# Kernel tuning notes

Hardware: AMD Instinct MI355X
Metric: run time of the kernel (lower is better)

## Reference

```python
import jax, jax.numpy as jnp
import numpy as np

B, T, P = 64, 512, 8
V, O, E, H, C_SIZE = 50000, 50000, 512, 2048, 5
A1, A2, A3, A4, A5 = 1.0, 0.5, 0.5, 0.5, 0.5


def setup_inputs() -> dict:
    key = jax.random.key(0)
    ks = jax.random.split(key, 8)
    s = 0.02
    return dict(
        encoder_output=jax.random.normal(ks[0], (B, H), jnp.float32),
        predict_sequence=jax.random.randint(ks[1], (B, P), 0, 500),
        source=jax.random.randint(ks[2], (B, T), 0, 500),
        source_lens=jax.random.randint(ks[3], (B,), T // 2, T + 1),
        E_table=jax.random.normal(ks[4], (V, E), jnp.float32) * s,
        W1=jax.random.normal(ks[5], (C_SIZE * E, H), jnp.float32) * s,
        b1=jnp.zeros((H,), jnp.float32),
        W2=jax.random.normal(ks[6], (H, O), jnp.float32) * s,
        b2=jnp.zeros((O,), jnp.float32),
        W3=jax.random.normal(ks[7], (H, O), jnp.float32) * s,
        b3=jnp.zeros((O,), jnp.float32),
    )


def _features(predict_sequence, source, source_lens):
    # Vectorized replacement of the per-sample Python n-gram/reorder loop.
    b, t = source.shape
    mask = jnp.arange(t)[None, :] < source_lens[:, None]          # valid positions [B,T]
    w1 = predict_sequence[:, -1]                                  # last predicted token
    w2a = predict_sequence[:, -2]                                 # second-to-last
    # bigram: exists p with source[p]==w1 and source[p+1]==source[pos]
    first2 = source[:, :-1] == w1[:, None]                        # [B,T-1]
    eq2 = source[:, :, None] == source[:, None, 1:]               # [B,T,T-1]
    big = jnp.any(eq2 & first2[:, None, :], axis=-1)              # [B,T]
    # trigram: exists p with source[p]==w2a, source[p+1]==w1, source[p+2]==source[pos]
    first3 = (source[:, :-2] == w2a[:, None]) & (source[:, 1:-1] == w1[:, None])
    eq3 = source[:, :, None] == source[:, None, 2:]               # [B,T,T-2]
    tri = jnp.any(eq3 & first3[:, None, :], axis=-1)
    # reordering: first index of source[pos] < first index of w1 (when w1 present)
    eqw = source == w1[:, None]
    in_list = jnp.any(eqw, axis=-1)
    kpos = jnp.argmax(eqw, axis=-1)                               # first occurrence of w1
    jpos = jnp.argmax(source[:, :, None] == source[:, None, :], axis=-1)  # first occ. of each id
    reo = in_list[:, None] & (jpos < kpos[:, None])
    rows = jnp.broadcast_to(jnp.arange(b)[:, None], (b, t))
    def scat(flags):
        return jnp.zeros((b, O), jnp.float32).at[rows, source].max((flags & mask).astype(jnp.float32))
    return scat(mask), scat(big), scat(tri), scat(reo)


def reference(encoder_output, predict_sequence, source, source_lens,
              E_table, W1, b1, W2, b2, W3, b3):
    bsz = encoder_output.shape[0]
    ctx = E_table[predict_sequence[:, -C_SIZE:]].reshape(bsz, -1)  # [B, C*E]
    h = jnp.tanh(ctx @ W1 + b1)                                    # [B, H]
    out = (h @ W2 + b2) + (encoder_output @ W3 + b3)               # Vh + Wenc
    uni, big, tri, reo = _features(predict_sequence, source, source_lens)
    comb = out * A1 + uni * A2 + big * A3 + tri * A4 + reo * A5
    return jax.nn.softmax(comb, axis=1)
```

## Files before the change

### kernel.cpp

```cpp
#include <hip/hip_runtime.h>
#include <math.h>

#define BSZ   64
#define TLEN  512
#define ODIM  50000
#define HDIM  2048
#define K1DIM 2560
#define K2DIM 4096
#define KSPLIT 5

typedef __bf16 bf16x8 __attribute__((ext_vector_type(8)));
typedef float f32x4 __attribute__((ext_vector_type(4)));

__device__ __forceinline__ unsigned short f2b(float f) {
    unsigned int u = __float_as_uint(f);
    u += 0x7FFFu + ((u >> 16) & 1u);
    return (unsigned short)(u >> 16);
}

__device__ __forceinline__ bf16x8 ld_bf16x8(const unsigned short* p) {
    union { uint4 u; bf16x8 v; } x;
    x.u = *reinterpret_cast<const uint4*>(p);
    return x.v;
}

__global__ __launch_bounds__(256) void prep_kernel(
    const float* __restrict__ enc, const int* __restrict__ ps,
    const float* __restrict__ Et, unsigned short* __restrict__ ctx,
    unsigned short* __restrict__ A2)
{
    int i = blockIdx.x * 256 + threadIdx.x;
    const int NE = BSZ * HDIM;
    if (i < NE) {
        int m = i >> 11, j = i & (HDIM - 1);
        A2[m * K2DIM + HDIM + j] = f2b(enc[i]);
    } else {
        int t = i - NE;
        int m = t / K1DIM, j = t - m * K1DIM;
        int c = j >> 9, e = j & 511;
        int tok = ps[m * 8 + 3 + c];
        ctx[m * K1DIM + j] = f2b(Et[(size_t)tok * 512 + e]);
    }
}

__global__ __launch_bounds__(256) void gemm1_kernel(
    const unsigned short* __restrict__ Actx, const float* __restrict__ W1,
    float* __restrict__ part)
{
    int n0 = blockIdx.x * 64;
    int ks = blockIdx.y;
    int wave = threadIdx.x >> 6;
    int lane = threadIdx.x & 63;
    int q = lane >> 4, l16 = lane & 15;
    int ncol = n0 + wave * 16 + l16;

    f32x4 acc[4] = {};
    for (int kk = 0; kk < 16; ++kk) {
        int kq = ks * 512 + kk * 32 + q * 8;
        const unsigned short* ap = Actx + l16 * K1DIM + kq;
        bf16x8 a0 = ld_bf16x8(ap);
        bf16x8 a1 = ld_bf16x8(ap + 16 * K1DIM);
        bf16x8 a2 = ld_bf16x8(ap + 32 * K1DIM);
        bf16x8 a3 = ld_bf16x8(ap + 48 * K1DIM);
        const float* wp = W1 + (size_t)kq * HDIM + ncol;
        union { unsigned short s[8]; bf16x8 v; } bb;
#pragma unroll
        for (int j = 0; j < 8; ++j) { bb.s[j] = f2b(*wp); wp += HDIM; }
        acc[0] = __builtin_amdgcn_mfma_f32_16x16x32_bf16(a0, bb.v, acc[0], 0, 0, 0);
        acc[1] = __builtin_amdgcn_mfma_f32_16x16x32_bf16(a1, bb.v, acc[1], 0, 0, 0);
        acc[2] = __builtin_amdgcn_mfma_f32_16x16x32_bf16(a2, bb.v, acc[2], 0, 0, 0);
        acc[3] = __builtin_amdgcn_mfma_f32_16x16x32_bf16(a3, bb.v, acc[3], 0, 0, 0);
    }
    float* pp = part + (size_t)ks * (BSZ * HDIM);
#pragma unroll
    for (int mt = 0; mt < 4; ++mt)
#pragma unroll
        for (int r = 0; r < 4; ++r)
            pp[(mt * 16 + q * 4 + r) * HDIM + ncol] = acc[mt][r];
}

__global__ __launch_bounds__(256) void htanh_kernel(
    const float* __restrict__ part, const float* __restrict__ b1,
    unsigned short* __restrict__ A2)
{
    int i = blockIdx.x * 256 + threadIdx.x;
    int m = i >> 11, n = i & (HDIM - 1);
    float s = b1[n];
#pragma unroll
    for (int ks = 0; ks < KSPLIT; ++ks) s += part[(size_t)ks * (BSZ * HDIM) + m * HDIM + n];
    A2[m * K2DIM + n] = f2b(tanhf(s));
}

#define KT 64
#define SKB 136
#define BUFB (KT * SKB)

__global__ __launch_bounds__(256) void gemm2_kernel(
    const unsigned short* __restrict__ A, const float* __restrict__ W2,
    const float* __restrict__ W3, const float* __restrict__ b2,
    const float* __restrict__ b3, float* __restrict__ out)
{
    __shared__ char lds[2 * BUFB];
    int bid = blockIdx.x;
    int tile = (bid & 7) * 98 + (bid >> 3);
    if (tile >= 782) return;
    int n0 = tile * 64;

    int tid = threadIdx.x;
    int wave = tid >> 6;
    int lane = tid & 63;
    int q = lane >> 4, l16 = lane & 15;
    int ncol = n0 + wave * 16 + l16;
    int nloc = wave * 16 + l16;

    int rr = tid >> 4;
    int cg = tid & 15;
    int gcol = n0 + cg * 4;
    if (gcol > ODIM - 4) gcol = ODIM - 4;

    float4 Sa[4], Sb[4];
    f32x4 acc[4] = {};
    const unsigned short* abase = A + l16 * K2DIM;
    char* buf0 = lds;
    char* buf1 = lds + BUFB;

#define ISSUE(S, ktile) do {                                                  \
    int kg0 = (ktile) * KT;                                                   \
    _Pragma("unroll")                                                         \
    for (int r = 0; r < 4; ++r) {                                             \
        int krow = kg0 + r * 16 + rr;                                         \
        const float* srcp = (krow < HDIM) ? (W2 + (size_t)krow * ODIM)        \
                                          : (W3 + (size_t)(krow - HDIM) * ODIM); \
        S[r] = *reinterpret_cast<const float4*>(srcp + gcol);                 \
    } } while (0)

#define CONVERT(S, bufc) do {                                                 \
    _Pragma("unroll")                                                         \
    for (int r = 0; r < 4; ++r) {                                             \
        union { unsigned short s[4]; unsigned long long u; } pk;              \
        pk.s[0] = f2b(S[r].x); pk.s[1] = f2b(S[r].y);                         \
        pk.s[2] = f2b(S[r].z); pk.s[3] = f2b(S[r].w);                         \
        *reinterpret_cast<unsigned long long*>((bufc) + (r * 16 + rr) * SKB + cg * 8) = pk.u; \
    } } while (0)

#define COMPUTE(bufc, ktile) do {                                             \
    _Pragma("unroll")                                                         \
    for (int h = 0; h < 2; ++h) {                                             \
        int kq = (ktile) * KT + h * 32 + q * 8;                               \
        const unsigned short* ap = abase + kq;                                \
        bf16x8 a0 = ld_bf16x8(ap);                                            \
        bf16x8 a1 = ld_bf16x8(ap + 16 * K2DIM);                               \
        bf16x8 a2 = ld_bf16x8(ap + 32 * K2DIM);                               \
        bf16x8 a3 = ld_bf16x8(ap + 48 * K2DIM);                               \
        union { unsigned short s[8]; bf16x8 v; } bb;                          \
        const char* bp = (bufc) + (h * 32 + q * 8) * SKB + nloc * 2;          \
        _Pragma("unroll")                                                     \
        for (int j = 0; j < 8; ++j)                                           \
            bb.s[j] = *reinterpret_cast<const unsigned short*>(bp + j * SKB); \
        acc[0] = __builtin_amdgcn_mfma_f32_16x16x32_bf16(a0, bb.v, acc[0], 0, 0, 0); \
        acc[1] = __builtin_amdgcn_mfma_f32_16x16x32_bf16(a1, bb.v, acc[1], 0, 0, 0); \
        acc[2] = __builtin_amdgcn_mfma_f32_16x16x32_bf16(a2, bb.v, acc[2], 0, 0, 0); \
        acc[3] = __builtin_amdgcn_mfma_f32_16x16x32_bf16(a3, bb.v, acc[3], 0, 0, 0); \
    } } while (0)

#define BARRIER do {                                                          \
    asm volatile("s_waitcnt lgkmcnt(0)" ::: "memory");                        \
    __builtin_amdgcn_s_barrier();                                             \
} while (0)

    ISSUE(Sa, 0);
    ISSUE(Sb, 1);
    asm volatile("s_waitcnt vmcnt(4)" ::: "memory");
    CONVERT(Sa, buf0);
    BARRIER;

    for (int kt = 0; kt < 62; kt += 2) {
        ISSUE(Sa, kt + 2);
        asm volatile("s_waitcnt vmcnt(4)" ::: "memory");
        CONVERT(Sb, buf1);
        COMPUTE(buf0, kt);
        BARRIER;

        ISSUE(Sb, kt + 3);
        asm volatile("s_waitcnt vmcnt(4)" ::: "memory");
        CONVERT(Sa, buf0);
        COMPUTE(buf1, kt + 1);
        BARRIER;
    }
    asm volatile("s_waitcnt vmcnt(0)" ::: "memory");
    CONVERT(Sb, buf1);
    COMPUTE(buf0, 62);
    BARRIER;
    COMPUTE(buf1, 63);

#undef ISSUE
#undef CONVERT
#undef COMPUTE
#undef BARRIER

    if (ncol < ODIM) {
        float bias = b2[ncol] + b3[ncol];
#pragma unroll
        for (int mt = 0; mt < 4; ++mt)
#pragma unroll
            for (int r = 0; r < 4; ++r)
                out[(size_t)(mt * 16 + q * 4 + r) * ODIM + ncol] = acc[mt][r] + bias;
    }
}

__global__ __launch_bounds__(256) void feats_kernel(
    const int* __restrict__ src_g, const int* __restrict__ lens,
    const int* __restrict__ ps, float* __restrict__ out)
{
    __shared__ int src[TLEN];
    int b = blockIdx.x;
    int tid = threadIdx.x;
    for (int t = tid; t < TLEN; t += 256) src[t] = src_g[b * TLEN + t];
    __syncthreads();
    int len = lens[b];
    int w1 = ps[b * 8 + 7];
    int w2a = ps[b * 8 + 6];

    for (int t = tid; t < TLEN; t += 256) {
        int v = src[t];
        bool first = true, big = false, tri = false;
        int kp = TLEN;
        for (int j = 0; j < TLEN; ++j) {
            int sj = src[j];
            int sj1 = (j < TLEN - 1) ? src[j + 1] : -1;
            int sj2 = (j < TLEN - 2) ? src[j + 2] : -1;
            if (j < t && sj == v) first = false;
            if (sj == w1 && sj1 == v) big = true;
            if (sj == w2a && sj1 == w1 && sj2 == v) tri = true;
            if (sj == w1 && j < kp) kp = j;
        }
        if (t < len && first) {
            bool in_list = kp < TLEN;
            bool reo = in_list && (t < kp);
            float add = 0.5f * (1.0f + (big ? 1.0f : 0.0f) + (tri ? 1.0f : 0.0f) + (reo ? 1.0f : 0.0f));
            out[(size_t)b * ODIM + v] += add;
        }
    }
}

__global__ __launch_bounds__(256) void rowstats_kernel(
    const float* __restrict__ out, float* __restrict__ stats)
{
    int b = blockIdx.x, tid = threadIdx.x;
    const float* row = out + (size_t)b * ODIM;
    float m = -INFINITY, s = 0.0f;
    for (int i = tid; i < ODIM; i += 256) {
        float x = row[i];
        if (x > m) { s = s * __expf(m - x) + 1.0f; m = x; }
        else s += __expf(x - m);
    }
    __shared__ float ms[256], ss[256];
    ms[tid] = m; ss[tid] = s;
    __syncthreads();
    for (int off = 128; off > 0; off >>= 1) {
        if (tid < off) {
            float m1 = ms[tid], s1 = ss[tid];
            float m2 = ms[tid + off], s2 = ss[tid + off];
            float M = fmaxf(m1, m2);
            ss[tid] = s1 * __expf(m1 - M) + s2 * __expf(m2 - M);
            ms[tid] = M;
        }
        __syncthreads();
    }
    if (tid == 0) { stats[b] = ms[0]; stats[64 + b] = ss[0]; }
}

__global__ __launch_bounds__(256) void norm_kernel(
    float* __restrict__ out, const float* __restrict__ stats)
{
    int i = blockIdx.x * 256 + threadIdx.x;
    int row = i / 12500;
    int off = i - row * 12500;
    float m = stats[row];
    float inv = 1.0f / stats[64 + row];
    float4* p = reinterpret_cast<float4*>(out + (size_t)row * ODIM) + off;
    float4 x = *p;
    x.x = __expf(x.x - m) * inv;
    x.y = __expf(x.y - m) * inv;
    x.z = __expf(x.z - m) * inv;
    x.w = __expf(x.w - m) * inv;
    *p = x;
}

extern "C" void kernel_launch(void* const* d_in, const int* in_sizes, int n_in,
                              void* d_out, int out_size, void* d_ws, size_t ws_size,
                              hipStream_t stream) {
    const float* enc  = (const float*)d_in[0];
    const int*   ps   = (const int*)d_in[1];
    const int*   src  = (const int*)d_in[2];
    const int*   lens = (const int*)d_in[3];
    const float* Et   = (const float*)d_in[4];
    const float* W1   = (const float*)d_in[5];
    const float* b1   = (const float*)d_in[6];
    const float* W2   = (const float*)d_in[7];
    const float* b2   = (const float*)d_in[8];
    const float* W3   = (const float*)d_in[9];
    const float* b3   = (const float*)d_in[10];
    float* out = (float*)d_out;

    char* ws = (char*)d_ws;
    unsigned short* ctx = (unsigned short*)(ws);
    unsigned short* A2  = (unsigned short*)(ws + 524288);
    float* part         = (float*)(ws + 1048576);
    float* stats        = (float*)(ws + 3801088);

    prep_kernel<<<1152, 256, 0, stream>>>(enc, ps, Et, ctx, A2);
    gemm1_kernel<<<dim3(32, KSPLIT), 256, 0, stream>>>(ctx, W1, part);
    htanh_kernel<<<512, 256, 0, stream>>>(part, b1, A2);
    gemm2_kernel<<<784, 256, 0, stream>>>(A2, W2, W3, b2, b3, out);
    feats_kernel<<<64, 256, 0, stream>>>(src, lens, ps, out);
    rowstats_kernel<<<64, 256, 0, stream>>>(out, stats);
    norm_kernel<<<3125, 256, 0, stream>>>(out, stats);
}
```

Baseline: 1.188 ms.

## Widen gemm2 tiles to 128 columns with swizzled LDS and split feats blocks

Gemm2 now has each block cover 128 output columns instead of 64, so every wave computes two 16-column MFMA subtiles and reuses its A fragments twice. The grid shrinks from 784 to 391 blocks and the tile-to-XCD mapping changes to match. The LDS row stride grows and an XOR swizzle is applied to the B tile to limit bank conflicts, and twice as many float4 loads are kept in flight per stage. Feats_kernel is split into 4 chunks per batch row across 256 blocks of 128 threads to spread its serial scan over more CUs. The trade-off is more registers and LDS per block, and with 391 blocks the MI355X's CUs may not all be filled.

```diff
diff --git a/kernel.cpp b/kernel.cpp
--- a/kernel.cpp
+++ b/kernel.cpp
@@ -92,7 +92,7 @@
 }
 
 #define KT 64
-#define SKB 136
+#define SKB 264
 #define BUFB (KT * SKB)
 
 __global__ __launch_bounds__(256) void gemm2_kernel(
@@ -102,24 +102,22 @@
 {
     __shared__ char lds[2 * BUFB];
     int bid = blockIdx.x;
-    int tile = (bid & 7) * 98 + (bid >> 3);
-    if (tile >= 782) return;
-    int n0 = tile * 64;
+    int xcd = bid & 7, idx = bid >> 3;
+    int tile = (xcd < 7 ? xcd * 49 : 343) + idx;
+    int n0 = tile * 128;
 
     int tid = threadIdx.x;
     int wave = tid >> 6;
     int lane = tid & 63;
     int q = lane >> 4, l16 = lane & 15;
-    int ncol = n0 + wave * 16 + l16;
-    int nloc = wave * 16 + l16;
-
-    int rr = tid >> 4;
-    int cg = tid & 15;
+
+    int rr = tid >> 5;
+    int cg = tid & 31;
     int gcol = n0 + cg * 4;
     if (gcol > ODIM - 4) gcol = ODIM - 4;
 
-    float4 Sa[4], Sb[4];
-    f32x4 acc[4] = {};
+    float4 Sa[8], Sb[8];
+    f32x4 acc[4][2] = {};
     const unsigned short* abase = A + l16 * K2DIM;
     char* buf0 = lds;
     char* buf1 = lds + BUFB;
@@ -127,20 +125,22 @@
 #define ISSUE(S, ktile) do {                                                  \
     int kg0 = (ktile) * KT;                                                   \
     _Pragma("unroll")                                                         \
-    for (int r = 0; r < 4; ++r) {                                             \
-        int krow = kg0 + r * 16 + rr;                                         \
+    for (int r8 = 0; r8 < 8; ++r8) {                                          \
+        int krow = kg0 + r8 * 8 + rr;                                         \
         const float* srcp = (krow < HDIM) ? (W2 + (size_t)krow * ODIM)        \
                                           : (W3 + (size_t)(krow - HDIM) * ODIM); \
-        S[r] = *reinterpret_cast<const float4*>(srcp + gcol);                 \
+        S[r8] = *reinterpret_cast<const float4*>(srcp + gcol);                \
     } } while (0)
 
 #define CONVERT(S, bufc) do {                                                 \
     _Pragma("unroll")                                                         \
-    for (int r = 0; r < 4; ++r) {                                             \
+    for (int r8 = 0; r8 < 8; ++r8) {                                          \
+        int row = r8 * 8 + rr;                                                \
         union { unsigned short s[4]; unsigned long long u; } pk;              \
-        pk.s[0] = f2b(S[r].x); pk.s[1] = f2b(S[r].y);                         \
-        pk.s[2] = f2b(S[r].z); pk.s[3] = f2b(S[r].w);                         \
-        *reinterpret_cast<unsigned long long*>((bufc) + (r * 16 + rr) * SKB + cg * 8) = pk.u; \
+        pk.s[0] = f2b(S[r8].x); pk.s[1] = f2b(S[r8].y);                       \
+        pk.s[2] = f2b(S[r8].z); pk.s[3] = f2b(S[r8].w);                       \
+        *reinterpret_cast<unsigned long long*>(                               \
+            (bufc) + row * SKB + ((cg * 8) ^ ((row & 16) << 1))) = pk.u;      \
     } } while (0)
 
 #define COMPUTE(bufc, ktile) do {                                             \
@@ -152,15 +152,21 @@
         bf16x8 a1 = ld_bf16x8(ap + 16 * K2DIM);                               \
         bf16x8 a2 = ld_bf16x8(ap + 32 * K2DIM);                               \
         bf16x8 a3 = ld_bf16x8(ap + 48 * K2DIM);                               \
-        union { unsigned short s[8]; bf16x8 v; } bb;                          \
-        const char* bp = (bufc) + (h * 32 + q * 8) * SKB + nloc * 2;          \
+        int rbase = h * 32 + q * 8;                                           \
+        const char* bp0 = (bufc) + rbase * SKB;                               \
+        int xo = (rbase & 16) << 1;                                           \
         _Pragma("unroll")                                                     \
-        for (int j = 0; j < 8; ++j)                                           \
-            bb.s[j] = *reinterpret_cast<const unsigned short*>(bp + j * SKB); \
-        acc[0] = __builtin_amdgcn_mfma_f32_16x16x32_bf16(a0, bb.v, acc[0], 0, 0, 0); \
-        acc[1] = __builtin_amdgcn_mfma_f32_16x16x32_bf16(a1, bb.v, acc[1], 0, 0, 0); \
-        acc[2] = __builtin_amdgcn_mfma_f32_16x16x32_bf16(a2, bb.v, acc[2], 0, 0, 0); \
-        acc[3] = __builtin_amdgcn_mfma_f32_16x16x32_bf16(a3, bb.v, acc[3], 0, 0, 0); \
+        for (int sub = 0; sub < 2; ++sub) {                                   \
+            union { unsigned short s[8]; bf16x8 v; } bb;                      \
+            const char* bp = bp0 + (((wave * 32 + sub * 16 + l16) * 2) ^ xo); \
+            _Pragma("unroll")                                                 \
+            for (int j = 0; j < 8; ++j)                                       \
+                bb.s[j] = *reinterpret_cast<const unsigned short*>(bp + j * SKB); \
+            acc[0][sub] = __builtin_amdgcn_mfma_f32_16x16x32_bf16(a0, bb.v, acc[0][sub], 0, 0, 0); \
+            acc[1][sub] = __builtin_amdgcn_mfma_f32_16x16x32_bf16(a1, bb.v, acc[1][sub], 0, 0, 0); \
+            acc[2][sub] = __builtin_amdgcn_mfma_f32_16x16x32_bf16(a2, bb.v, acc[2][sub], 0, 0, 0); \
+            acc[3][sub] = __builtin_amdgcn_mfma_f32_16x16x32_bf16(a3, bb.v, acc[3][sub], 0, 0, 0); \
+        }                                                                     \
     } } while (0)
 
 #define BARRIER do {                                                          \
@@ -170,19 +176,19 @@
 
     ISSUE(Sa, 0);
     ISSUE(Sb, 1);
-    asm volatile("s_waitcnt vmcnt(4)" ::: "memory");
+    asm volatile("s_waitcnt vmcnt(8)" ::: "memory");
     CONVERT(Sa, buf0);
     BARRIER;
 
     for (int kt = 0; kt < 62; kt += 2) {
         ISSUE(Sa, kt + 2);
-        asm volatile("s_waitcnt vmcnt(4)" ::: "memory");
+        asm volatile("s_waitcnt vmcnt(8)" ::: "memory");
         CONVERT(Sb, buf1);
         COMPUTE(buf0, kt);
         BARRIER;
 
         ISSUE(Sb, kt + 3);
-        asm volatile("s_waitcnt vmcnt(4)" ::: "memory");
+        asm volatile("s_waitcnt vmcnt(8)" ::: "memory");
         CONVERT(Sa, buf0);
         COMPUTE(buf1, kt + 1);
         BARRIER;
@@ -198,48 +204,52 @@
 #undef COMPUTE
 #undef BARRIER
 
-    if (ncol < ODIM) {
-        float bias = b2[ncol] + b3[ncol];
-#pragma unroll
-        for (int mt = 0; mt < 4; ++mt)
-#pragma unroll
-            for (int r = 0; r < 4; ++r)
-                out[(size_t)(mt * 16 + q * 4 + r) * ODIM + ncol] = acc[mt][r] + bias;
-    }
-}
-
-__global__ __launch_bounds__(256) void feats_kernel(
+#pragma unroll
+    for (int sub = 0; sub < 2; ++sub) {
+        int ncol = n0 + wave * 32 + sub * 16 + l16;
+        if (ncol < ODIM) {
+            float bias = b2[ncol] + b3[ncol];
+#pragma unroll
+            for (int mt = 0; mt < 4; ++mt)
+#pragma unroll
+                for (int r = 0; r < 4; ++r)
+                    out[(size_t)(mt * 16 + q * 4 + r) * ODIM + ncol] = acc[mt][sub][r] + bias;
+        }
+    }
+}
+
+__global__ __launch_bounds__(128) void feats_kernel(
     const int* __restrict__ src_g, const int* __restrict__ lens,
     const int* __restrict__ ps, float* __restrict__ out)
 {
     __shared__ int src[TLEN];
-    int b = blockIdx.x;
+    int b = blockIdx.x >> 2;
+    int chunk = blockIdx.x & 3;
     int tid = threadIdx.x;
-    for (int t = tid; t < TLEN; t += 256) src[t] = src_g[b * TLEN + t];
+    for (int t = tid; t < TLEN; t += 128) src[t] = src_g[b * TLEN + t];
     __syncthreads();
     int len = lens[b];
     int w1 = ps[b * 8 + 7];
     int w2a = ps[b * 8 + 6];
 
-    for (int t = tid; t < TLEN; t += 256) {
-        int v = src[t];
-        bool first = true, big = false, tri = false;
-        int kp = TLEN;
-        for (int j = 0; j < TLEN; ++j) {
-            int sj = src[j];
-            int sj1 = (j < TLEN - 1) ? src[j + 1] : -1;
-            int sj2 = (j < TLEN - 2) ? src[j + 2] : -1;
-            if (j < t && sj == v) first = false;
-            if (sj == w1 && sj1 == v) big = true;
-            if (sj == w2a && sj1 == w1 && sj2 == v) tri = true;
-            if (sj == w1 && j < kp) kp = j;
-        }
-        if (t < len && first) {
-            bool in_list = kp < TLEN;
-            bool reo = in_list && (t < kp);
-            float add = 0.5f * (1.0f + (big ? 1.0f : 0.0f) + (tri ? 1.0f : 0.0f) + (reo ? 1.0f : 0.0f));
-            out[(size_t)b * ODIM + v] += add;
-        }
+    int t = chunk * 128 + tid;
+    int v = src[t];
+    bool first = true, big = false, tri = false;
+    int kp = TLEN;
+    for (int j = 0; j < TLEN; ++j) {
+        int sj = src[j];
+        int sj1 = (j < TLEN - 1) ? src[j + 1] : -1;
+        int sj2 = (j < TLEN - 2) ? src[j + 2] : -1;
+        if (j < t && sj == v) first = false;
+        if (sj == w1 && sj1 == v) big = true;
+        if (sj == w2a && sj1 == w1 && sj2 == v) tri = true;
+        if (sj == w1 && j < kp) kp = j;
+    }
+    if (t < len && first) {
+        bool in_list = kp < TLEN;
+        bool reo = in_list && (t < kp);
+        float add = 0.5f * (1.0f + (big ? 1.0f : 0.0f) + (tri ? 1.0f : 0.0f) + (reo ? 1.0f : 0.0f));
+        out[(size_t)b * ODIM + v] += add;
     }
 }
 
@@ -312,8 +322,8 @@
     prep_kernel<<<1152, 256, 0, stream>>>(enc, ps, Et, ctx, A2);
     gemm1_kernel<<<dim3(32, KSPLIT), 256, 0, stream>>>(ctx, W1, part);
     htanh_kernel<<<512, 256, 0, stream>>>(part, b1, A2);
-    gemm2_kernel<<<784, 256, 0, stream>>>(A2, W2, W3, b2, b3, out);
-    feats_kernel<<<64, 256, 0, stream>>>(src, lens, ps, out);
+    gemm2_kernel<<<391, 256, 0, stream>>>(A2, W2, W3, b2, b3, out);
+    feats_kernel<<<256, 128, 0, stream>>>(src, lens, ps, out);
     rowstats_kernel<<<64, 256, 0, stream>>>(out, stats);
     norm_kernel<<<3125, 256, 0, stream>>>(out, stats);
 }
```

After: 1.042 ms. 12.3% less time.
